# Optimization experiments

Hardware: AMD Instinct MI355X
Metric: run time of the kernel (lower is better)

Reference implementation:

```python
import jax, jax.numpy as jnp
import numpy as np

B, S, DIM, E, K = 8, 8192, 512, 4, 2
EPS = 1e-6


def setup_inputs() -> dict:
    key = jax.random.key(0)
    ks = jax.random.split(key, 4)
    scale = 0.02
    return {
        "x": jax.random.normal(ks[0], (B, S, DIM), dtype=jnp.float32),
        "router_w": jax.random.normal(ks[1], (DIM, E), dtype=jnp.float32) * scale,
        "router_b": jnp.zeros((E,), jnp.float32),
        "expert_w": jax.random.normal(ks[2], (E, DIM, DIM), dtype=jnp.float32) * scale,
        "expert_b": jnp.zeros((E, DIM), jnp.float32),
        "out_w": jax.random.normal(ks[3], (DIM, DIM), dtype=jnp.float32) * scale,
        "out_b": jnp.zeros((DIM,), jnp.float32),
        "norm_w": jnp.ones((DIM,), jnp.float32),
    }


def reference(x, router_w, router_b, expert_w, expert_b, out_w, out_b, norm_w):
    b, s, d = x.shape
    # router
    logits = x @ router_w + router_b                      # [B,S,E]
    topw, topi = jax.lax.top_k(logits, K)                 # [B,S,K]
    topw = jax.nn.softmax(topw, axis=-1)
    t = b * s
    xf = x.reshape(t, d)
    idx = topi.reshape(t, K)
    w = topw.reshape(t, K).astype(x.dtype)
    # dense token-expert weight mask (topk indices are distinct per token)
    mask = jnp.zeros((t, E), x.dtype).at[jnp.arange(t)[:, None], idx].set(w)
    # expert FFN: Linear + SiLU (dropout disabled in eval)
    h = jax.nn.silu(jnp.einsum("td,edh->teh", xf, expert_w) + expert_b)  # [T,E,D]
    comb = jnp.einsum("te,teh->th", mask, h)              # weighted combine
    out = comb @ out_w + out_b
    y = xf + out                                          # residual
    rms = jnp.sqrt(jnp.mean(y * y, axis=-1, keepdims=True) + EPS)
    return (norm_w * (y / rms)).reshape(b, s, d)
```

## Files before the change

### kernel.cpp

```cpp
#include <hip/hip_runtime.h>
#include <hip/hip_bf16.h>
#include <stdint.h>

#define NTOK 65536
#define DIM 512
#define NEXP 4
#define REG 14336

using u16 = unsigned short;
using u32 = unsigned int;
typedef __attribute__((ext_vector_type(4))) float f32x4;
typedef __attribute__((ext_vector_type(8))) short bf16x8;
typedef __attribute__((ext_vector_type(8))) u16 u16x8;
typedef __attribute__((ext_vector_type(4))) u16 u16x4;

__device__ __forceinline__ u16 f2bf(float f) {
  u32 u = __builtin_bit_cast(u32, f);
  u32 r = (u + 0x7FFFu + ((u >> 16) & 1u)) >> 16;
  return (u16)r;
}
__device__ __forceinline__ float bf2f(u16 v) {
  return __builtin_bit_cast(float, (u32)v << 16);
}

#define GLOAD_LDS16(gp, lp)                                                    \
  __builtin_amdgcn_global_load_lds(                                            \
      (const __attribute__((address_space(1))) void*)(gp),                     \
      (__attribute__((address_space(3))) void*)(lp), 16, 0, 0)

#define FENCE asm volatile("" ::: "memory")
#define BARRIER { FENCE; __builtin_amdgcn_s_barrier(); FENCE; }
#define LGKM0 { asm volatile("s_waitcnt lgkmcnt(0)" ::: "memory"); __builtin_amdgcn_sched_barrier(0); }
#define VMCNT_(n) asm volatile("s_waitcnt vmcnt(" #n ")" ::: "memory")
#define VMCNT(n) VMCNT_(n)
#define SB __builtin_amdgcn_sched_barrier(0)

__device__ __forceinline__ const bf16x8* lds_frag(const u16* base, int row, int chunk) {
  return (const bf16x8*)((const char*)base + row * 128 + (((chunk) ^ (row & 7)) << 4));
}
__device__ __forceinline__ const bf16x8* frag32(const u16* base, int row, int rchByte) {
  return (const bf16x8*)((const char*)base + row * 64 + rchByte);
}

__global__ void ewpack(const float* __restrict__ ew, u16* __restrict__ ewtp,
                       int* __restrict__ cnt) {
  if (blockIdx.x == 0 && threadIdx.x < 6) cnt[threadIdx.x] = 0;
  int lane = threadIdx.x & 63, wv = threadIdx.x >> 6;
  int f = blockIdx.x * 4 + wv;
  int hs = f & 31, T = (f >> 5) & 15, e = f >> 9;
  int r16 = lane & 15, lg = lane >> 4;
  int h = hs * 16 + r16;
  int d0 = T * 32 + lg * 8;
  u16x8 o;
#pragma unroll
  for (int q = 0; q < 8; ++q)
    o[q] = f2bf(ew[((size_t)e * DIM + d0 + q) * DIM + h]);
  *(u16x8*)(ewtp + (size_t)f * 512 + lane * 8) = o;
}

__global__ void owpack(const float* __restrict__ ow, u16* __restrict__ owt3) {
  int lane = threadIdx.x & 63, wv = threadIdx.x >> 6;
  int frag = blockIdx.x * 4 + wv;
  int j = frag & 7, kc = (frag >> 3) & 1, t = (frag >> 4) & 7, strip = frag >> 7;
  int r16 = lane & 15, lg = lane >> 4;
  int h = strip * 128 + j * 16 + r16;
  int d0 = t * 64 + kc * 32 + lg * 8;
  u16x8 o;
#pragma unroll
  for (int q = 0; q < 8; ++q) o[q] = f2bf(ow[(size_t)(d0 + q) * DIM + h]);
  *(u16x8*)(owt3 + (size_t)frag * 512 + lane * 8) = o;
}

__global__ void router_kernel(const float* __restrict__ x, const float* __restrict__ rw,
                              const float* __restrict__ rb, u16* __restrict__ xb,
                              int* __restrict__ pp, float2* __restrict__ wab) {
  int lane = threadIdx.x & 63, wave = threadIdx.x >> 6;
  size_t t = (size_t)blockIdx.x * 4 + wave;
  const float* xr = x + t * DIM + lane * 8;
  f32x4 v0 = *(const f32x4*)xr;
  f32x4 v1 = *(const f32x4*)(xr + 4);
  float l0 = 0.f, l1 = 0.f, l2 = 0.f, l3 = 0.f;
  const float* rwp = rw + (size_t)lane * 32;
#pragma unroll
  for (int j = 0; j < 8; ++j) {
    float xv = (j < 4) ? v0[j] : v1[j - 4];
    f32x4 r = *(const f32x4*)(rwp + j * 4);
    l0 += xv * r[0]; l1 += xv * r[1]; l2 += xv * r[2]; l3 += xv * r[3];
  }
#pragma unroll
  for (int off = 32; off; off >>= 1) {
    l0 += __shfl_xor(l0, off); l1 += __shfl_xor(l1, off);
    l2 += __shfl_xor(l2, off); l3 += __shfl_xor(l3, off);
  }
  float lv[4] = {l0 + rb[0], l1 + rb[1], l2 + rb[2], l3 + rb[3]};
  int i0 = 0; float b0 = lv[0];
#pragma unroll
  for (int e = 1; e < 4; ++e) if (lv[e] > b0) { b0 = lv[e]; i0 = e; }
  int i1 = (i0 == 0) ? 1 : 0; float b1 = lv[i1];
#pragma unroll
  for (int e = 0; e < 4; ++e) if (e != i0 && lv[e] > b1) { b1 = lv[e]; i1 = e; }
  float ex = __expf(b1 - b0);
  float w0 = 1.0f / (1.0f + ex);
  float w1 = ex * w0;
  if (lane == 0) {
    int a = (i0 < i1) ? i0 : i1;
    int b = (i0 < i1) ? i1 : i0;
    const int ptab[16] = {-1, 0, 1, 2, -1, -1, 3, 4, -1, -1, -1, 5, -1, -1, -1, -1};
    pp[t] = ptab[a * 4 + b];
    float wa = (a == i0) ? w0 : w1;
    float wb = (a == i0) ? w1 : w0;
    wab[t] = make_float2(wa, wb);
  }
  u16x8 o;
#pragma unroll
  for (int j = 0; j < 4; ++j) { o[j] = f2bf(v0[j]); o[4 + j] = f2bf(v1[j]); }
  *(u16x8*)(xb + t * DIM + lane * 8) = o;
}

__global__ void assignscatter(const int* __restrict__ pp, const float2* __restrict__ wab,
                              int* __restrict__ cnt, int* __restrict__ list,
                              float2* __restrict__ wpair) {
  int t = blockIdx.x * 256 + threadIdx.x;
  int lane = threadIdx.x & 63;
  int p = pp[t];
  float2 w = wab[t];
  int pos = 0;
#pragma unroll
  for (int q = 0; q < 6; ++q) {
    unsigned long long m = __ballot(p == q);
    if (p == q) {
      int rank = __popcll(m & ((1ull << lane) - 1ull));
      int leader = __ffsll((long long)m) - 1;
      int base = 0;
      if (lane == leader) base = atomicAdd(&cnt[q], (int)__popcll(m));
      base = __shfl(base, leader);
      pos = base + rank;
    }
  }
  int slot = p * REG + pos;
  if (pos < REG) {
    list[slot] = t;
    wpair[slot] = w;
  }
}

__global__ __launch_bounds__(256, 2) void expert_gemm(
    const u16* __restrict__ xb, const u16* __restrict__ ewtp,
    const float* __restrict__ ebias, const int* __restrict__ cnt,
    const int* __restrict__ list, const float2* __restrict__ wpair,
    u16* __restrict__ comb) {
  __shared__ u16 Asl[3][128 * 32];
  int tid = threadIdx.x, lane = tid & 63, wave = tid >> 6;
  int wy = wave >> 1, wx = wave & 1;
  int b = blockIdx.x;
  int chunk = b >> 5, within = b & 31;
  int panel = chunk * 8 + (within & 7);
  int nblk = within >> 3;
  int p = panel / (REG / 128);
  int m0 = panel * 128;
  int cntp = cnt[p];
  if (m0 - p * REG >= cntp) return;
  int n0 = nblk * 128;
  const int ea2[6] = {0, 0, 0, 1, 1, 2};
  const int eb2[6] = {1, 2, 3, 2, 3, 3};
  int eA = ea2[p], eB = eb2[p];

  int r4 = lane >> 2, c4 = lane & 3;
  int rot = (r4 >> 1) & 3;
  int kch = ((c4 - rot) & 3) * 8;
  int r16 = lane & 15, lg = lane >> 4;
  int rchB = (((lg + ((r16 >> 1) & 3)) & 3)) * 16;

  int sid2[2];
#pragma unroll
  for (int j = 0; j < 2; ++j) {
    int slot = m0 + wave * 32 + j * 16 + r4;
    int idv = list[slot];
    sid2[j] = ((slot - p * REG) < cntp) ? idv : 0;
  }
  const u16* a0b = xb + (size_t)sid2[0] * DIM + kch;
  const u16* a1b = xb + (size_t)sid2[1] * DIM + kch;
  const u16* bpA = ewtp + (size_t)eA * 262144 + (size_t)(n0 / 16 + wx * 4) * 512 + lane * 8;
  const u16* bpB = ewtp + (size_t)eB * 262144 + (size_t)(n0 / 16 + wx * 4) * 512 + lane * 8;

  f32x4 accA[4][4], accB[4][4];
#pragma unroll
  for (int i = 0; i < 4; ++i)
#pragma unroll
    for (int j = 0; j < 4; ++j) { accA[i][j] = (f32x4)(0.f); accB[i][j] = (f32x4)(0.f); }

#define STAGE(BI, KS)                                                          \
  do {                                                                         \
    GLOAD_LDS16(a0b + (KS) * 32, Asl[BI] + (wave * 32) * 32);                  \
    GLOAD_LDS16(a1b + (KS) * 32, Asl[BI] + (wave * 32 + 16) * 32);             \
  } while (0)
#define LOADBX(BV, S)                                                          \
  do {                                                                         \
    _Pragma("unroll") for (int i = 0; i < 4; ++i) {                            \
      BV[i]     = *(const bf16x8*)(bpA + (S) * 16384 + i * 512);               \
      BV[4 + i] = *(const bf16x8*)(bpB + (S) * 16384 + i * 512);               \
    }                                                                          \
  } while (0)

  bf16x8 BE[8], BO[8];
  STAGE(0, 0); SB;
  STAGE(1, 1); SB;
  LOADBX(BE, 0); SB;
  VMCNT(10);
  BARRIER;

#define KST(T, BC, BN, WC)                                                     \
  {                                                                            \
    if ((T) + 1 < 16) { LOADBX(BN, (T) + 1); }                                 \
    SB;                                                                        \
    if ((T) + 2 < 16) { STAGE(((T) + 2) % 3, (T) + 2); }                       \
    SB;                                                                        \
    bf16x8 a[4];                                                               \
    _Pragma("unroll") for (int i = 0; i < 4; ++i)                              \
      a[i] = *frag32(Asl[(T) % 3], wy * 64 + i * 16 + r16, rchB);              \
    __builtin_amdgcn_s_setprio(1);                                             \
    _Pragma("unroll") for (int i = 0; i < 4; ++i)                              \
      _Pragma("unroll") for (int j = 0; j < 4; ++j)                            \
        accA[i][j] = __builtin_amdgcn_mfma_f32_16x16x32_bf16(a[i], BC[j], accA[i][j], 0, 0, 0); \
    _Pragma("unroll") for (int i = 0; i < 4; ++i)                              \
      _Pragma("unroll") for (int j = 0; j < 4; ++j)                            \
        accB[i][j] = __builtin_amdgcn_mfma_f32_16x16x32_bf16(a[i], BC[4 + j], accB[i][j], 0, 0, 0); \
    __builtin_amdgcn_s_setprio(0);                                             \
    WC;                                                                        \
  }

  KST(0,  BE, BO, { VMCNT(2); BARRIER; })
  KST(1,  BO, BE, { VMCNT(2); BARRIER; })
  KST(2,  BE, BO, { VMCNT(2); BARRIER; })
  KST(3,  BO, BE, { VMCNT(2); BARRIER; })
  KST(4,  BE, BO, { VMCNT(2); BARRIER; })
  KST(5,  BO, BE, { VMCNT(2); BARRIER; })
  KST(6,  BE, BO, { VMCNT(2); BARRIER; })
  KST(7,  BO, BE, { VMCNT(2); BARRIER; })
  KST(8,  BE, BO, { VMCNT(2); BARRIER; })
  KST(9,  BO, BE, { VMCNT(2); BARRIER; })
  KST(10, BE, BO, { VMCNT(2); BARRIER; })
  KST(11, BO, BE, { VMCNT(2); BARRIER; })
  KST(12, BE, BO, { VMCNT(2); BARRIER; })
  KST(13, BO, BE, { VMCNT(2); BARRIER; })
  KST(14, BE, BO, { VMCNT(2); BARRIER; })
  KST(15, BO, BE, {})
#undef KST
#undef LOADBX
#undef STAGE

  float bA4[4], bB4[4];
#pragma unroll
  for (int j = 0; j < 4; ++j) {
    int h = n0 + wx * 64 + j * 16 + r16;
    bA4[j] = ebias[eA * DIM + h];
    bB4[j] = ebias[eB * DIM + h];
  }
#pragma unroll
  for (int i = 0; i < 4; ++i) {
    int rb = wy * 64 + i * 16 + lg * 4;
#pragma unroll
    for (int rr = 0; rr < 4; ++rr) {
      int slot = m0 + rb + rr;
      bool val = (slot - p * REG) < cntp;
      int id = list[slot];
      float2 wv = wpair[slot];
#pragma unroll
      for (int j = 0; j < 4; ++j) {
        float zA = accA[i][j][rr] + bA4[j];
        float zB = accB[i][j][rr] + bB4[j];
        float sA = zA / (1.0f + __expf(-zA));
        float sB = zB / (1.0f + __expf(-zB));
        float v = wv.x * sA + wv.y * sB;
        if (val) {
          int h = n0 + wx * 64 + j * 16 + r16;
          comb[(size_t)id * DIM + h] = f2bf(v);
        }
      }
    }
  }
}

__global__ __launch_bounds__(256, 2) void outnorm(
    const u16* __restrict__ comb, const u16* __restrict__ owt3,
    const float* __restrict__ ob, const u16* __restrict__ xb,
    const float* __restrict__ nw, float* __restrict__ out) {
  __shared__ u16 As[3][64 * 64];
  __shared__ float rowsum[64][4];
  int tid = threadIdx.x, lane = tid & 63, w = tid >> 6;
  int m0 = blockIdx.x * 64;
  int r16 = lane & 15, lg = lane >> 4;
  int rl = lane >> 3;
  int scb = ((lane & 7) ^ rl) * 8;
  int n0w = w * 128;

  f32x4 acc[8][4];
#pragma unroll
  for (int j = 0; j < 8; ++j)
#pragma unroll
    for (int i = 0; i < 4; ++i) acc[j][i] = (f32x4)(0.f);

#define OSTG(bi, ks)                                                           \
  _Pragma("unroll") for (int jj = 0; jj < 2; ++jj) {                           \
    GLOAD_LDS16(comb + (size_t)(m0 + w * 16 + jj * 8 + rl) * DIM + (ks) * 64 + scb, \
                As[bi] + (w * 16 + jj * 8) * 64);                              \
  }
#define LOADB(BV, HH)                                                          \
  {                                                                            \
    const u16* bp_ = owt3 +                                                    \
        ((size_t)(((w * 8 + ((HH) >> 1)) * 2 + ((HH) & 1)) * 8)) * 512 + lane * 8; \
    _Pragma("unroll") for (int jj = 0; jj < 8; ++jj)                           \
      BV[jj] = *(const bf16x8*)(bp_ + jj * 512);                               \
  }
#define HSTEP(H, BC, BN, WC)                                                   \
  {                                                                            \
    if (((H) & 1) == 0 && ((H) >> 1) + 2 < 8) OSTG((((H) >> 1) + 2) % 3, ((H) >> 1) + 2); \
    if ((H) + 1 < 16) LOADB(BN, (H) + 1);                                      \
    bf16x8 af[4];                                                              \
    _Pragma("unroll") for (int ii = 0; ii < 4; ++ii)                           \
      af[ii] = *lds_frag(As[((H) >> 1) % 3], ii * 16 + r16, ((H) & 1) * 4 + lg); \
    LGKM0;                                                                     \
    __builtin_amdgcn_s_setprio(1);                                             \
    _Pragma("unroll") for (int jj = 0; jj < 8; ++jj)                           \
      _Pragma("unroll") for (int ii = 0; ii < 4; ++ii)                         \
        acc[jj][ii] = __builtin_amdgcn_mfma_f32_16x16x32_bf16(BC[jj], af[ii], acc[jj][ii], 0, 0, 0); \
    __builtin_amdgcn_s_setprio(0);                                             \
    WC;                                                                        \
  }

  bf16x8 BE[8], BO[8];
  OSTG(0, 0); OSTG(1, 1);
  LOADB(BE, 0);
  VMCNT(10);
  BARRIER;

  HSTEP(0,  BE, BO, {})
  HSTEP(1,  BO, BE, { VMCNT(10); BARRIER; })
  HSTEP(2,  BE, BO, {})
  HSTEP(3,  BO, BE, { VMCNT(10); BARRIER; })
  HSTEP(4,  BE, BO, {})
  HSTEP(5,  BO, BE, { VMCNT(10); BARRIER; })
  HSTEP(6,  BE, BO, {})
  HSTEP(7,  BO, BE, { VMCNT(10); BARRIER; })
  HSTEP(8,  BE, BO, {})
  HSTEP(9,  BO, BE, { VMCNT(10); BARRIER; })
  HSTEP(10, BE, BO, {})
  HSTEP(11, BO, BE, { VMCNT(10); BARRIER; })
  HSTEP(12, BE, BO, {})
  HSTEP(13, BO, BE, { VMCNT(8); BARRIER; })
  HSTEP(14, BE, BO, {})
  HSTEP(15, BO, BE, {})
#undef HSTEP
#undef LOADB
#undef OSTG

  float part[4] = {0.f, 0.f, 0.f, 0.f};
#pragma unroll
  for (int hj = 0; hj < 8; ++hj) {
    int h0 = n0w + hj * 16 + lg * 4;
    f32x4 obv = *(const f32x4*)(ob + h0);
#pragma unroll
    for (int ti = 0; ti < 4; ++ti) {
      int t = m0 + ti * 16 + r16;
      u16x4 xv4 = *(const u16x4*)(xb + (size_t)t * DIM + h0);
#pragma unroll
      for (int rr = 0; rr < 4; ++rr) {
        float yv = bf2f(xv4[rr]) + acc[hj][ti][rr] + obv[rr];
        acc[hj][ti][rr] = yv;
        part[ti] += yv * yv;
      }
    }
  }
#pragma unroll
  for (int ti = 0; ti < 4; ++ti) {
    part[ti] += __shfl_xor(part[ti], 16);
    part[ti] += __shfl_xor(part[ti], 32);
  }
  if (lane < 16) {
#pragma unroll
    for (int ti = 0; ti < 4; ++ti) rowsum[ti * 16 + r16][w] = part[ti];
  }
  __syncthreads();
  float inv[4];
#pragma unroll
  for (int ti = 0; ti < 4; ++ti) {
    int tr = ti * 16 + r16;
    float s = rowsum[tr][0] + rowsum[tr][1] + rowsum[tr][2] + rowsum[tr][3];
    inv[ti] = 1.0f / sqrtf(s * (1.0f / 512.0f) + 1e-6f);
  }
#pragma unroll
  for (int hj = 0; hj < 8; ++hj) {
    int h0 = n0w + hj * 16 + lg * 4;
    f32x4 nwv = *(const f32x4*)(nw + h0);
#pragma unroll
    for (int ti = 0; ti < 4; ++ti) {
      int t = m0 + ti * 16 + r16;
      f32x4 o;
#pragma unroll
      for (int rr = 0; rr < 4; ++rr) o[rr] = acc[hj][ti][rr] * inv[ti] * nwv[rr];
      *(f32x4*)(out + (size_t)t * DIM + h0) = o;
    }
  }
}

extern "C" void kernel_launch(void* const* d_in, const int* in_sizes, int n_in,
                              void* d_out, int out_size, void* d_ws, size_t ws_size,
                              hipStream_t stream) {
  const float* x  = (const float*)d_in[0];
  const float* rw = (const float*)d_in[1];
  const float* rb = (const float*)d_in[2];
  const float* ew = (const float*)d_in[3];
  const float* eb = (const float*)d_in[4];
  const float* ow = (const float*)d_in[5];
  const float* ob = (const float*)d_in[6];
  const float* nw = (const float*)d_in[7];
  float* out = (float*)d_out;

  char* ws = (char*)d_ws;
  u16*   xb    = (u16*)(ws);
  u16*   combb = (u16*)(ws + 67108864);
  int*   pp    = (int*)(ws + 67108864);
  float2* wab  = (float2*)(ws + 67108864 + 262144);
  u16*   ewtp  = (u16*)(ws + 134217728);
  u16*   owt3  = (u16*)(ws + 136314880);
  int*   list  = (int*)(ws + 136839168);
  float2* wpair = (float2*)(ws + 136839168 + 344064);
  int*   cnt   = (int*)(ws + 136839168 + 344064 + 688128);

  ewpack<<<512, 256, 0, stream>>>(ew, ewtp, cnt);
  owpack<<<128, 256, 0, stream>>>(ow, owt3);
  router_kernel<<<NTOK / 4, 256, 0, stream>>>(x, rw, rb, xb, pp, wab);
  assignscatter<<<NTOK / 256, 256, 0, stream>>>(pp, wab, cnt, list, wpair);
  expert_gemm<<<dim3(6 * REG / 128 * 4), 256, 0, stream>>>(xb, ewtp, eb, cnt, list, wpair, combb);
  outnorm<<<dim3(NTOK / 64), 256, 0, stream>>>(combb, owt3, ob, xb, nw, out);
}
```

Measured before the change: 321.7 us.

## Widen expert GEMM K-step to 64 and merge weight-pack kernels

The expert GEMM now stages 64-wide K slices of gathered token rows into LDS (four 16-byte global-to-LDS loads per wave, new XOR swizzle), halving the number of pipeline stages and barriers from 16 to 8. B fragments are no longer double-buffered across steps; both K-halves are loaded at the start of each step. The two weight-packing kernels are fused into one launch. This trades fewer barriers and a launch for doubled LDS use and less prefetch overlap of the B loads, which may expose global latency.

```diff
diff --git a/kernel.cpp b/kernel.cpp
--- a/kernel.cpp
+++ b/kernel.cpp
@@ -38,37 +38,32 @@
 __device__ __forceinline__ const bf16x8* lds_frag(const u16* base, int row, int chunk) {
   return (const bf16x8*)((const char*)base + row * 128 + (((chunk) ^ (row & 7)) << 4));
 }
-__device__ __forceinline__ const bf16x8* frag32(const u16* base, int row, int rchByte) {
-  return (const bf16x8*)((const char*)base + row * 64 + rchByte);
-}
-
-__global__ void ewpack(const float* __restrict__ ew, u16* __restrict__ ewtp,
-                       int* __restrict__ cnt) {
+
+__global__ void packw(const float* __restrict__ ew, const float* __restrict__ ow,
+                      u16* __restrict__ ewtp, u16* __restrict__ owt3,
+                      int* __restrict__ cnt) {
   if (blockIdx.x == 0 && threadIdx.x < 6) cnt[threadIdx.x] = 0;
   int lane = threadIdx.x & 63, wv = threadIdx.x >> 6;
-  int f = blockIdx.x * 4 + wv;
-  int hs = f & 31, T = (f >> 5) & 15, e = f >> 9;
+  int gf = blockIdx.x * 4 + wv;
   int r16 = lane & 15, lg = lane >> 4;
-  int h = hs * 16 + r16;
-  int d0 = T * 32 + lg * 8;
   u16x8 o;
-#pragma unroll
-  for (int q = 0; q < 8; ++q)
-    o[q] = f2bf(ew[((size_t)e * DIM + d0 + q) * DIM + h]);
-  *(u16x8*)(ewtp + (size_t)f * 512 + lane * 8) = o;
-}
-
-__global__ void owpack(const float* __restrict__ ow, u16* __restrict__ owt3) {
-  int lane = threadIdx.x & 63, wv = threadIdx.x >> 6;
-  int frag = blockIdx.x * 4 + wv;
-  int j = frag & 7, kc = (frag >> 3) & 1, t = (frag >> 4) & 7, strip = frag >> 7;
-  int r16 = lane & 15, lg = lane >> 4;
-  int h = strip * 128 + j * 16 + r16;
-  int d0 = t * 64 + kc * 32 + lg * 8;
-  u16x8 o;
-#pragma unroll
-  for (int q = 0; q < 8; ++q) o[q] = f2bf(ow[(size_t)(d0 + q) * DIM + h]);
-  *(u16x8*)(owt3 + (size_t)frag * 512 + lane * 8) = o;
+  if (gf < 2048) {
+    int hs = gf & 31, T = (gf >> 5) & 15, e = gf >> 9;
+    int h = hs * 16 + r16;
+    int d0 = T * 32 + lg * 8;
+#pragma unroll
+    for (int q = 0; q < 8; ++q)
+      o[q] = f2bf(ew[((size_t)e * DIM + d0 + q) * DIM + h]);
+    *(u16x8*)(ewtp + (size_t)gf * 512 + lane * 8) = o;
+  } else {
+    int frag = gf - 2048;
+    int j = frag & 7, kc = (frag >> 3) & 1, t = (frag >> 4) & 7, strip = frag >> 7;
+    int h = strip * 128 + j * 16 + r16;
+    int d0 = t * 64 + kc * 32 + lg * 8;
+#pragma unroll
+    for (int q = 0; q < 8; ++q) o[q] = f2bf(ow[(size_t)(d0 + q) * DIM + h]);
+    *(u16x8*)(owt3 + (size_t)frag * 512 + lane * 8) = o;
+  }
 }
 
 __global__ void router_kernel(const float* __restrict__ x, const float* __restrict__ rw,
@@ -149,7 +144,7 @@
     const float* __restrict__ ebias, const int* __restrict__ cnt,
     const int* __restrict__ list, const float2* __restrict__ wpair,
     u16* __restrict__ comb) {
-  __shared__ u16 Asl[3][128 * 32];
+  __shared__ u16 Asl[3][128 * 64];
   int tid = threadIdx.x, lane = tid & 63, wave = tid >> 6;
   int wy = wave >> 1, wx = wave & 1;
   int b = blockIdx.x;
@@ -165,21 +160,24 @@
   const int eb2[6] = {1, 2, 3, 2, 3, 3};
   int eA = ea2[p], eB = eb2[p];
 
-  int r4 = lane >> 2, c4 = lane & 3;
-  int rot = (r4 >> 1) & 3;
-  int kch = ((c4 - rot) & 3) * 8;
   int r16 = lane & 15, lg = lane >> 4;
-  int rchB = (((lg + ((r16 >> 1) & 3)) & 3)) * 16;
-
-  int sid2[2];
-#pragma unroll
-  for (int j = 0; j < 2; ++j) {
-    int slot = m0 + wave * 32 + j * 16 + r4;
+  int rl = lane >> 3;
+  int scb = ((lane & 7) ^ rl) * 8;
+  int s = r16 & 7;
+  int ab0 = (wy * 64 + r16) * 128 + ((s >> 2) << 6) + ((lg ^ (s & 3)) << 4);
+  int ab1 = ab0 ^ 64;
+
+  int sid[4];
+#pragma unroll
+  for (int j = 0; j < 4; ++j) {
+    int slot = m0 + wave * 32 + j * 8 + rl;
     int idv = list[slot];
-    sid2[j] = ((slot - p * REG) < cntp) ? idv : 0;
-  }
-  const u16* a0b = xb + (size_t)sid2[0] * DIM + kch;
-  const u16* a1b = xb + (size_t)sid2[1] * DIM + kch;
+    sid[j] = ((slot - p * REG) < cntp) ? idv : 0;
+  }
+  const u16* a0b = xb + (size_t)sid[0] * DIM + scb;
+  const u16* a1b = xb + (size_t)sid[1] * DIM + scb;
+  const u16* a2b = xb + (size_t)sid[2] * DIM + scb;
+  const u16* a3b = xb + (size_t)sid[3] * DIM + scb;
   const u16* bpA = ewtp + (size_t)eA * 262144 + (size_t)(n0 / 16 + wx * 4) * 512 + lane * 8;
   const u16* bpB = ewtp + (size_t)eB * 262144 + (size_t)(n0 / 16 + wx * 4) * 512 + lane * 8;
 
@@ -191,62 +189,67 @@
 
 #define STAGE(BI, KS)                                                          \
   do {                                                                         \
-    GLOAD_LDS16(a0b + (KS) * 32, Asl[BI] + (wave * 32) * 32);                  \
-    GLOAD_LDS16(a1b + (KS) * 32, Asl[BI] + (wave * 32 + 16) * 32);             \
+    GLOAD_LDS16(a0b + (KS) * 64, Asl[BI] + (wave * 32) * 64);                  \
+    GLOAD_LDS16(a1b + (KS) * 64, Asl[BI] + (wave * 32 + 8) * 64);              \
+    GLOAD_LDS16(a2b + (KS) * 64, Asl[BI] + (wave * 32 + 16) * 64);             \
+    GLOAD_LDS16(a3b + (KS) * 64, Asl[BI] + (wave * 32 + 24) * 64);             \
   } while (0)
-#define LOADBX(BV, S)                                                          \
+#define LOADB(BV, T32)                                                         \
   do {                                                                         \
     _Pragma("unroll") for (int i = 0; i < 4; ++i) {                            \
-      BV[i]     = *(const bf16x8*)(bpA + (S) * 16384 + i * 512);               \
-      BV[4 + i] = *(const bf16x8*)(bpB + (S) * 16384 + i * 512);               \
+      BV[i]     = *(const bf16x8*)(bpA + (T32) * 16384 + i * 512);             \
+      BV[4 + i] = *(const bf16x8*)(bpB + (T32) * 16384 + i * 512);             \
     }                                                                          \
   } while (0)
 
-  bf16x8 BE[8], BO[8];
   STAGE(0, 0); SB;
   STAGE(1, 1); SB;
-  LOADBX(BE, 0); SB;
-  VMCNT(10);
+  VMCNT(4);
   BARRIER;
 
-#define KST(T, BC, BN, WC)                                                     \
+  bf16x8 Bk0[8], Bk1[8];
+#define KST(T, WC)                                                             \
   {                                                                            \
-    if ((T) + 1 < 16) { LOADBX(BN, (T) + 1); }                                 \
+    LOADB(Bk0, 2 * (T));                                                       \
+    LOADB(Bk1, 2 * (T) + 1);                                                   \
     SB;                                                                        \
-    if ((T) + 2 < 16) { STAGE(((T) + 2) % 3, (T) + 2); }                       \
+    if ((T) + 2 < 8) { STAGE(((T) + 2) % 3, (T) + 2); }                        \
     SB;                                                                        \
+    const char* Ab_ = (const char*)Asl[(T) % 3];                               \
     bf16x8 a[4];                                                               \
     _Pragma("unroll") for (int i = 0; i < 4; ++i)                              \
-      a[i] = *frag32(Asl[(T) % 3], wy * 64 + i * 16 + r16, rchB);              \
+      a[i] = *(const bf16x8*)(Ab_ + ab0 + i * 2048);                           \
     __builtin_amdgcn_s_setprio(1);                                             \
     _Pragma("unroll") for (int i = 0; i < 4; ++i)                              \
       _Pragma("unroll") for (int j = 0; j < 4; ++j)                            \
-        accA[i][j] = __builtin_amdgcn_mfma_f32_16x16x32_bf16(a[i], BC[j], accA[i][j], 0, 0, 0); \
+        accA[i][j] = __builtin_amdgcn_mfma_f32_16x16x32_bf16(a[i], Bk0[j], accA[i][j], 0, 0, 0); \
     _Pragma("unroll") for (int i = 0; i < 4; ++i)                              \
       _Pragma("unroll") for (int j = 0; j < 4; ++j)                            \
-        accB[i][j] = __builtin_amdgcn_mfma_f32_16x16x32_bf16(a[i], BC[4 + j], accB[i][j], 0, 0, 0); \
+        accB[i][j] = __builtin_amdgcn_mfma_f32_16x16x32_bf16(a[i], Bk0[4 + j], accB[i][j], 0, 0, 0); \
+    __builtin_amdgcn_s_setprio(0);                                             \
+    _Pragma("unroll") for (int i = 0; i < 4; ++i)                              \
+      a[i] = *(const bf16x8*)(Ab_ + ab1 + i * 2048);                           \
+    __builtin_amdgcn_s_setprio(1);                                             \
+    _Pragma("unroll") for (int i = 0; i < 4; ++i)                              \
+      _Pragma("unroll") for (int j = 0; j < 4; ++j)                            \
+        accA[i][j] = __builtin_amdgcn_mfma_f32_16x16x32_bf16(a[i], Bk1[j], accA[i][j], 0, 0, 0); \
+    _Pragma("unroll") for (int i = 0; i < 4; ++i)                              \
+      _Pragma("unroll") for (int j = 0; j < 4; ++j)                            \
+        accB[i][j] = __builtin_amdgcn_mfma_f32_16x16x32_bf16(a[i], Bk1[4 + j], accB[i][j], 0, 0, 0); \
     __builtin_amdgcn_s_setprio(0);                                             \
     WC;                                                                        \
   }
 
-  KST(0,  BE, BO, { VMCNT(2); BARRIER; })
-  KST(1,  BO, BE, { VMCNT(2); BARRIER; })
-  KST(2,  BE, BO, { VMCNT(2); BARRIER; })
-  KST(3,  BO, BE, { VMCNT(2); BARRIER; })
-  KST(4,  BE, BO, { VMCNT(2); BARRIER; })
-  KST(5,  BO, BE, { VMCNT(2); BARRIER; })
-  KST(6,  BE, BO, { VMCNT(2); BARRIER; })
-  KST(7,  BO, BE, { VMCNT(2); BARRIER; })
-  KST(8,  BE, BO, { VMCNT(2); BARRIER; })
-  KST(9,  BO, BE, { VMCNT(2); BARRIER; })
-  KST(10, BE, BO, { VMCNT(2); BARRIER; })
-  KST(11, BO, BE, { VMCNT(2); BARRIER; })
-  KST(12, BE, BO, { VMCNT(2); BARRIER; })
-  KST(13, BO, BE, { VMCNT(2); BARRIER; })
-  KST(14, BE, BO, { VMCNT(2); BARRIER; })
-  KST(15, BO, BE, {})
+  KST(0, { VMCNT(4); BARRIER; })
+  KST(1, { VMCNT(4); BARRIER; })
+  KST(2, { VMCNT(4); BARRIER; })
+  KST(3, { VMCNT(4); BARRIER; })
+  KST(4, { VMCNT(4); BARRIER; })
+  KST(5, { VMCNT(4); BARRIER; })
+  KST(6, { VMCNT(0); BARRIER; })
+  KST(7, {})
 #undef KST
-#undef LOADBX
+#undef LOADB
 #undef STAGE
 
   float bA4[4], bB4[4];
@@ -427,8 +430,7 @@
   float2* wpair = (float2*)(ws + 136839168 + 344064);
   int*   cnt   = (int*)(ws + 136839168 + 344064 + 688128);
 
-  ewpack<<<512, 256, 0, stream>>>(ew, ewtp, cnt);
-  owpack<<<128, 256, 0, stream>>>(ow, owt3);
+  packw<<<640, 256, 0, stream>>>(ew, ow, ewtp, owt3, cnt);
   router_kernel<<<NTOK / 4, 256, 0, stream>>>(x, rw, rb, xb, pp, wab);
   assignscatter<<<NTOK / 256, 256, 0, stream>>>(pp, wab, cnt, list, wpair);
   expert_gemm<<<dim3(6 * REG / 128 * 4), 256, 0, stream>>>(xb, ewtp, eb, cnt, list, wpair, combb);
```

New measurement: 317.8 us (median of 2 runs). About the same (-1.2%).
